# Optimization experiments

Measured on AMD Instinct MI355X. Metric: run time of the kernel, lower is better.

The kernel has to match this reference:

```python
import jax, jax.numpy as jnp
import numpy as np

NEG = -1e9

def conv1x1(x, w, b):
    # x: [B,C,H,W], w: [O,C], b: [O]
    return jnp.einsum('bchw,oc->bohw', x, w) + b[None, :, None, None]


def setup_inputs() -> dict:
    key = jax.random.key(0)
    ks = jax.random.split(key, 12)
    B, C, H, W = 4, 512, 96, 96
    Cr = min(8, C // 8)  # = 8
    s = lambda fan: 1.0 / np.sqrt(fan)
    inp = {
        'x':   jax.random.normal(ks[0], (B, C, H, W), dtype=jnp.float32),
        'w_h': jax.random.normal(ks[1], (Cr, C), dtype=jnp.float32) * s(C),
        'b_h': jax.random.normal(ks[2], (Cr,), dtype=jnp.float32) * s(C),
        'w_w': jax.random.normal(ks[3], (Cr, C), dtype=jnp.float32) * s(C),
        'b_w': jax.random.normal(ks[4], (Cr,), dtype=jnp.float32) * s(C),
        'w_c': jax.random.normal(ks[5], (C, C), dtype=jnp.float32) * s(C),
        'b_c': jax.random.normal(ks[6], (C,), dtype=jnp.float32) * s(C),
        'w_o': jax.random.normal(ks[7], (C, C), dtype=jnp.float32) * s(C),
        'b_o': jax.random.normal(ks[8], (C,), dtype=jnp.float32) * s(C),
        # alpha/beta/gamma are nn.Parameter(zeros(1)); use small nonzero values
        # so all branches contribute to output/gradients.
        'alpha': jax.random.normal(ks[9], (1,), dtype=jnp.float32) * 0.1,
        'beta':  jax.random.normal(ks[10], (1,), dtype=jnp.float32) * 0.1,
        'gamma': jax.random.normal(ks[11], (1,), dtype=jnp.float32) * 0.1,
    }
    return inp


def reference(x, w_h, b_h, w_w, b_w, w_c, b_c, w_o, b_o, alpha, beta, gamma):
    B, C, H, W = x.shape
    f_hei = conv1x1(x, w_h, b_h)              # [B,Cr,H,W]
    Cr = f_hei.shape[1]
    # Faithful replication of torch permute/contiguous/view sequence
    # (the .view(B*W,-1,H) after permute reinterprets the (H,Cr) layout as (Cr,H)).
    f_h = f_hei.transpose(0, 3, 2, 1).reshape(B * W, Cr, H).transpose(0, 2, 1)  # [B*W,H,Cr]
    f_w = f_hei.transpose(0, 2, 1, 3).reshape(B * H, Cr, W).transpose(0, 2, 1)  # [B*H,W,Cr]
    f_wid = conv1x1(x, w_w, b_w)              # [B,Cr,H,W]
    ff_h = f_wid.transpose(0, 3, 1, 2).reshape(B * W, Cr, H)  # [B*W,Cr,H]
    ff_w = f_wid.transpose(0, 2, 1, 3).reshape(B * H, Cr, W)  # [B*H,Cr,W]
    # channel attention branch
    f_ch = conv1x1(x, w_c, b_c)               # [B,C,H,W]
    f_c = f_ch.reshape(B, C, H * W)           # [B,C,HW]
    ff_c = f_ch.transpose(0, 2, 3, 1).reshape(B, H * W, C)    # [B,HW,C]
    aff_c = jax.nn.softmax(jnp.matmul(f_c, ff_c), axis=2)     # [B,C,C]
    out_C = jnp.matmul(ff_c, aff_c).reshape(B, C, H, W)       # torch .view reinterpretation
    # axial (criss-cross) attention with masked concat-softmax
    E_h = jnp.matmul(f_h, ff_h)               # [B*W,H,H]
    E_h = E_h + (jnp.eye(H, dtype=x.dtype) * NEG)[None, :, :]
    E_h = E_h.reshape(B, W, H, H).transpose(0, 2, 1, 3)       # [B,H,W,H]
    E_w = jnp.matmul(f_w, ff_w).reshape(B, H, W, W)           # [B,H,W,W]
    concate = jax.nn.softmax(jnp.concatenate([E_h, E_w], axis=3), axis=3)  # [B,H,W,H+W]
    h_att = concate[:, :, :, :H].transpose(0, 2, 1, 3).reshape(B * W, H, H)
    w_att = concate[:, :, :, H:].reshape(B * H, W, W)
    f_cha = conv1x1(x, w_o, b_o)              # [B,C,H,W]
    P_H = f_cha.transpose(0, 3, 1, 2).reshape(B * W, C, H)
    P_W = f_cha.transpose(0, 2, 1, 3).reshape(B * H, C, W)
    out_H = jnp.matmul(P_H, h_att.transpose(0, 2, 1)).reshape(B, W, C, H).transpose(0, 2, 3, 1)
    out_W = jnp.matmul(P_W, w_att.transpose(0, 2, 1)).reshape(B, H, C, W).transpose(0, 2, 1, 3)
    return x + alpha * out_H + beta * out_W + gamma * out_C
```

## Files before the change

kernel.cpp:

```cpp
#include <hip/hip_runtime.h>

typedef __attribute__((ext_vector_type(8))) short short8;
typedef __attribute__((ext_vector_type(4))) float f32x4;
typedef __attribute__((ext_vector_type(4))) unsigned short us4;
typedef unsigned short u16;

#define kB 4
#define kC 512
#define kCr 8
#define kH 96
#define kW 96
#define kHW 9216
#define kCHW 4718592
#define NEGV -1e9f

__device__ __forceinline__ u16 f2b(float f) {
  union { float f; unsigned u; } v; v.f = f;
  unsigned r = v.u + 0x7fff + ((v.u >> 16) & 1);
  return (u16)(r >> 16);
}
__device__ __forceinline__ float b2f(u16 h) {
  union { unsigned u; float f; } v; v.u = ((unsigned)h) << 16;
  return v.f;
}
#define MFMA(a, b, c) __builtin_amdgcn_mfma_f32_16x16x32_bf16(a, b, c, 0, 0, 0)

__device__ __forceinline__ void gl16(const u16* g, u16* l) {
  __builtin_amdgcn_global_load_lds(
      (const __attribute__((address_space(1))) void*)g,
      (__attribute__((address_space(3))) void*)l, 16, 0, 0);
}

__global__ __launch_bounds__(256) void k_cvt_T(const float* __restrict__ in,
                                               u16* __restrict__ out,
                                               int R, int C) {
  const float* ib = in + (size_t)blockIdx.z * R * C;
  u16* ob = out + (size_t)blockIdx.z * R * C;
  int c0 = blockIdx.x * 64, r0 = blockIdx.y * 64;
  __shared__ u16 T[64][68];
  int tid = threadIdx.x;
#pragma unroll
  for (int p = 0; p < 4; p++) {
    int ch = tid + p * 256;
    int i = ch >> 4, seg = ch & 15;
    f32x4 v = *(const f32x4*)&ib[(size_t)(r0 + i) * C + c0 + seg * 4];
    T[i][seg*4+0] = f2b(v[0]); T[i][seg*4+1] = f2b(v[1]);
    T[i][seg*4+2] = f2b(v[2]); T[i][seg*4+3] = f2b(v[3]);
  }
  __syncthreads();
#pragma unroll
  for (int p = 0; p < 4; p++) {
    int ch = tid + p * 256;
    int j = ch >> 4, seg = ch & 15;
    us4 o;
#pragma unroll
    for (int e = 0; e < 4; e++) o[e] = T[seg*4+e][j];
    *(us4*)&ob[(size_t)(c0 + j) * R + r0 + seg * 4] = o;
  }
}

__global__ __launch_bounds__(256) void k_trT_bf(const u16* __restrict__ in,
                                                u16* __restrict__ out,
                                                int R, int C) {
  const u16* ib = in + (size_t)blockIdx.z * R * C;
  u16* ob = out + (size_t)blockIdx.z * R * C;
  int c0 = blockIdx.x * 64, r0 = blockIdx.y * 64;
  __shared__ u16 T[64][68];
  int tid = threadIdx.x;
#pragma unroll
  for (int p = 0; p < 4; p++) {
    int ch = tid + p * 256;
    int i = ch >> 4, seg = ch & 15;
    us4 v = *(const us4*)&ib[(size_t)(r0 + i) * C + c0 + seg * 4];
    T[i][seg*4+0] = v[0]; T[i][seg*4+1] = v[1];
    T[i][seg*4+2] = v[2]; T[i][seg*4+3] = v[3];
  }
  __syncthreads();
#pragma unroll
  for (int p = 0; p < 4; p++) {
    int ch = tid + p * 256;
    int j = ch >> 4, seg = ch & 15;
    us4 o;
#pragma unroll
    for (int e = 0; e < 4; e++) o[e] = T[seg*4+e][j];
    *(us4*)&ob[(size_t)(c0 + j) * R + r0 + seg * 4] = o;
  }
}

__global__ __launch_bounds__(256) void k_cvtw(const float* __restrict__ wc,
                                              const float* __restrict__ wo,
                                              u16* __restrict__ wco) {
  int i = blockIdx.x * 256 + threadIdx.x;
  const float* src = (i < 65536) ? &wc[(size_t)i * 4] : &wo[(size_t)(i - 65536) * 4];
  f32x4 v = *(const f32x4*)src;
  us4 o;
  o[0] = f2b(v[0]); o[1] = f2b(v[1]); o[2] = f2b(v[2]); o[3] = f2b(v[3]);
  ((us4*)wco)[i] = o;
}

__global__ __launch_bounds__(256) void k_conv16(
    const float* __restrict__ wh, const float* __restrict__ bh,
    const float* __restrict__ ww, const float* __restrict__ bw,
    const u16* __restrict__ XT, u16* __restrict__ Out) {
  __shared__ u16 As[16][520];
  __shared__ float bias_s[16];
  int tid = threadIdx.x;
#pragma unroll
  for (int p = 0; p < 4; p++) {
    int ch = tid + p * 256;
    int r = ch >> 6, seg = ch & 63;
    const float* src = (r < 8) ? &wh[r * 512 + seg * 8] : &ww[(r - 8) * 512 + seg * 8];
    f32x4 v0 = *(const f32x4*)src;
    f32x4 v1 = *(const f32x4*)(src + 4);
    short8 sv;
    sv[0]=f2b(v0[0]); sv[1]=f2b(v0[1]); sv[2]=f2b(v0[2]); sv[3]=f2b(v0[3]);
    sv[4]=f2b(v1[0]); sv[5]=f2b(v1[1]); sv[6]=f2b(v1[2]); sv[7]=f2b(v1[3]);
    *(short8*)&As[r][seg * 8] = sv;
  }
  if (tid < 16) bias_s[tid] = (tid < 8) ? bh[tid] : bw[tid - 8];
  __syncthreads();
  int b = blockIdx.y;
  int nb = blockIdx.x * 128 + (tid >> 6) * 32;
  int lane = tid & 63;
  int lr = lane & 15, lg = lane >> 4;
  const u16* Bb = XT + (size_t)b * kCHW;
  f32x4 acc[2] = {};
#pragma unroll 4
  for (int k0 = 0; k0 < 512; k0 += 32) {
    short8 a = *(const short8*)&As[lr][k0 + lg * 8];
    short8 b0 = *(const short8*)&Bb[(size_t)(nb + lr) * 512 + k0 + lg * 8];
    short8 b1 = *(const short8*)&Bb[(size_t)(nb + 16 + lr) * 512 + k0 + lg * 8];
    acc[0] = MFMA(a, b0, acc[0]);
    acc[1] = MFMA(a, b1, acc[1]);
  }
#pragma unroll
  for (int q = 0; q < 2; q++)
#pragma unroll
    for (int r = 0; r < 4; r++) {
      int m = lg * 4 + r;
      Out[((size_t)b * 16 + m) * kHW + nb + q * 16 + lr] = f2b(acc[q][r] + bias_s[m]);
    }
}

#define GEMM_PROLOG()                                                      \
  int tid = threadIdx.x;                                                   \
  int lane = tid & 63, wv = tid >> 6;                                      \
  int wr = (wv >> 1) * 64, wc = (wv & 1) * 64;                             \
  int lr = lane & 15, lg = lane >> 4;                                      \
  f32x4 acc[4][4] = {};

#define STAGE(bufv, kk)                                                    \
  {                                                                        \
    _Pragma("unroll")                                                      \
    for (int p = 0; p < 4; p++) {                                          \
      int ch = tid + p * 256;                                              \
      int row = ch >> 3, cc = ch & 7;                                      \
      int sc = (cc ^ (row & 7)) * 8;                                       \
      gl16(&Asrc[(size_t)(bm + row) * LDA + (kk) + sc], &As[bufv][row][cc * 8]); \
      gl16(&Bsrc[(size_t)(bn + row) * LDB + (kk) + sc], &Bs[bufv][row][cc * 8]); \
    }                                                                      \
  }

#define COMPUTE(bufv)                                                      \
  {                                                                        \
    _Pragma("unroll")                                                      \
    for (int ks = 0; ks < 2; ks++) {                                       \
      int ca = ((ks * 4 + lg) ^ (lr & 7)) * 8;                             \
      short8 av[4], bv[4];                                                 \
      _Pragma("unroll")                                                    \
      for (int m = 0; m < 4; m++)                                          \
        av[m] = *(const short8*)&As[bufv][wr + m * 16 + lr][ca];           \
      _Pragma("unroll")                                                    \
      for (int n = 0; n < 4; n++)                                          \
        bv[n] = *(const short8*)&Bs[bufv][wc + n * 16 + lr][ca];           \
      _Pragma("unroll")                                                    \
      for (int m = 0; m < 4; m++)                                          \
        _Pragma("unroll")                                                  \
        for (int n = 0; n < 4; n++)                                        \
          acc[m][n] = MFMA(av[m], bv[n], acc[m][n]);                       \
    }                                                                      \
  }

__global__ __launch_bounds__(256) void k_gemm_conv2(
    const u16* __restrict__ wco, const u16* __restrict__ BT,
    const float* __restrict__ b_c, const float* __restrict__ b_o,
    u16* __restrict__ f_ch, u16* __restrict__ f_cha) {
  __shared__ u16 As[2][128][64];
  __shared__ u16 Bs[2][128][64];
  int b = blockIdx.z;
  int bm = blockIdx.y * 128;
  int bn = blockIdx.x * 128;
  const u16* Asrc = wco;
  const u16* Bsrc = BT + (size_t)b * kCHW;
  const int LDA = 512, LDB = 512;
  GEMM_PROLOG();
  STAGE(0, 0);
  __syncthreads();
  int cur = 0;
#pragma unroll 1
  for (int t = 0; t < 7; t++) {
    STAGE(cur ^ 1, (t + 1) * 64);
    COMPUTE(cur);
    __syncthreads();
    cur ^= 1;
  }
  COMPUTE(cur);
  const float* biasp = (bm < 512) ? (b_c + bm) : (b_o + bm - 512);
  u16* Ob = (bm < 512) ? (f_ch + (size_t)b * kCHW + (size_t)bm * kHW)
                       : (f_cha + (size_t)b * kCHW + (size_t)(bm - 512) * kHW);
#pragma unroll
  for (int m = 0; m < 4; m++)
#pragma unroll
    for (int r = 0; r < 4; r++) {
      int ol = wr + m * 16 + lg * 4 + r;
      float bv_ = biasp[ol];
#pragma unroll
      for (int n = 0; n < 4; n++)
        Ob[(size_t)ol * kHW + bn + wc + n * 16 + lr] = f2b(acc[m][n][r] + bv_);
    }
}

__global__ __launch_bounds__(256) void k_gram_sk(const u16* __restrict__ F,
                                                 float* __restrict__ part) {
  __shared__ u16 As[2][128][64];
  __shared__ u16 Bs[2][128][64];
  int z = blockIdx.z;
  int b = z & 3, s = z >> 2;
  int bm = blockIdx.y * 128, bn = blockIdx.x * 128;
  const u16* Asrc = F + (size_t)b * kCHW;
  const u16* Bsrc = Asrc;
  const int LDA = kHW, LDB = kHW;
  int kbeg = s * 1152;
  GEMM_PROLOG();
  STAGE(0, kbeg);
  __syncthreads();
  int cur = 0;
#pragma unroll 1
  for (int t = 0; t < 17; t++) {
    STAGE(cur ^ 1, kbeg + (t + 1) * 64);
    COMPUTE(cur);
    __syncthreads();
    cur ^= 1;
  }
  COMPUTE(cur);
  float* Pb = part + ((size_t)(s * 4 + b)) * 262144;
#pragma unroll
  for (int m = 0; m < 4; m++)
#pragma unroll
    for (int r = 0; r < 4; r++) {
      int i = bm + wr + m * 16 + lg * 4 + r;
#pragma unroll
      for (int n = 0; n < 4; n++)
        Pb[(size_t)i * 512 + bn + wc + n * 16 + lr] = acc[m][n][r];
    }
}

__global__ __launch_bounds__(256) void k_outc(
    const u16* __restrict__ AT, const u16* __restrict__ Bt,
    const float* __restrict__ gamma, u16* __restrict__ Out) {
  __shared__ u16 As[2][128][64];
  __shared__ u16 Bs[2][128][64];
  int b = blockIdx.z;
  int bm = blockIdx.y * 128;
  int bn = blockIdx.x * 128;
  const u16* Asrc = AT + (size_t)b * kCHW;
  const u16* Bsrc = Bt + (size_t)b * 262144;
  const int LDA = 512, LDB = 512;
  GEMM_PROLOG();
  STAGE(0, 0);
  __syncthreads();
  int cur = 0;
#pragma unroll 1
  for (int t = 0; t < 7; t++) {
    STAGE(cur ^ 1, (t + 1) * 64);
    COMPUTE(cur);
    __syncthreads();
    cur ^= 1;
  }
  COMPUTE(cur);
  float g = *gamma;
  u16* Ob = Out + (size_t)b * kCHW;
#pragma unroll
  for (int m = 0; m < 4; m++)
#pragma unroll
    for (int r = 0; r < 4; r++) {
      int mm = bm + wr + m * 16 + lg * 4 + r;
#pragma unroll
      for (int n = 0; n < 4; n++)
        Ob[(size_t)mm * 512 + bn + wc + n * 16 + lr] = f2b(g * acc[m][n][r]);
    }
}

__global__ __launch_bounds__(256) void k_softmax512r(const float* __restrict__ part,
                                                     float* __restrict__ gramN) {
  int b = blockIdx.x >> 9, i = blockIdx.x & 511;
  int tid = threadIdx.x;
  float v0 = 0.f, v1 = 0.f;
#pragma unroll
  for (int s = 0; s < 8; s++) {
    const float* P = part + ((size_t)(s * 4 + b) * 512 + i) * 512;
    v0 += P[tid];
    v1 += P[tid + 256];
  }
  int wid = tid >> 6, lane = tid & 63;
  float m = fmaxf(v0, v1);
#pragma unroll
  for (int o = 32; o >= 1; o >>= 1) m = fmaxf(m, __shfl_xor(m, o));
  __shared__ float redm[4], reds[4];
  if (lane == 0) redm[wid] = m;
  __syncthreads();
  m = fmaxf(fmaxf(redm[0], redm[1]), fmaxf(redm[2], redm[3]));
  float e0 = expf(v0 - m), e1 = expf(v1 - m);
  float s = e0 + e1;
#pragma unroll
  for (int o = 32; o >= 1; o >>= 1) s += __shfl_xor(s, o);
  if (lane == 0) reds[wid] = s;
  __syncthreads();
  s = reds[0] + reds[1] + reds[2] + reds[3];
  float inv = 1.0f / s;
  float* R = gramN + ((size_t)b * 512 + i) * 512;
  R[tid] = e0 * inv;
  R[tid + 256] = e1 * inv;
}

__global__ __launch_bounds__(256) void k_eh(
    const u16* __restrict__ fhw, u16* __restrict__ Ccat) {
  int b = blockIdx.x / kW, w = blockIdx.x % kW;
  __shared__ float fh[kH][kCr];
  __shared__ float fw[kCr][kH];
  int tid = threadIdx.x;
  for (int l = tid; l < kH * kCr; l += 256) {
    int i = l >> 3, c = l & 7;
    fh[i][c] = b2f(fhw[((size_t)b * 16 + (i & 7)) * kHW + (c * 12 + (i >> 3)) * kW + w]);
    int c2 = l / kH, j = l % kH;
    fw[c2][j] = b2f(fhw[((size_t)b * 16 + 8 + c2) * kHW + j * kW + w]);
  }
  __syncthreads();
  for (int t = tid; t < kH * kH; t += 256) {
    int i = t / kH, j = t % kH;
    float e = 0.f;
#pragma unroll
    for (int c = 0; c < kCr; c++) e += fh[i][c] * fw[c][j];
    if (i == j) e += NEGV;
    Ccat[(((size_t)b * kH + i) * kW + w) * 192 + j] = f2b(e);
  }
}

__global__ __launch_bounds__(256) void k_ew(
    const u16* __restrict__ fhw, u16* __restrict__ Ccat) {
  int b = blockIdx.x / kH, h = blockIdx.x % kH;
  __shared__ float fh2[kCr][kW];
  __shared__ float fw2[kCr][kW];
  int tid = threadIdx.x;
  for (int l = tid; l < kCr * kW; l += 256) {
    int c = l / kW, w = l % kW;
    fh2[c][w] = b2f(fhw[((size_t)b * 16 + c) * kHW + h * kW + w]);
    fw2[c][w] = b2f(fhw[((size_t)b * 16 + 8 + c) * kHW + h * kW + w]);
  }
  __syncthreads();
  for (int t = tid; t < kW * kW; t += 256) {
    int w = t / kW, j = t % kW;
    float e = 0.f;
#pragma unroll
    for (int c = 0; c < kCr; c++) e += fh2[c][w] * fw2[c][j];
    Ccat[(((size_t)b * kH + h) * kW + w) * 192 + 96 + j] = f2b(e);
  }
}

__global__ __launch_bounds__(256) void k_softmax192(u16* __restrict__ Ccat) {
  int r = blockIdx.x * 4 + (threadIdx.x >> 6);
  int lane = threadIdx.x & 63;
  u16* R = Ccat + (size_t)r * 192;
  float a = b2f(R[lane]), b = b2f(R[lane + 64]), c = b2f(R[lane + 128]);
  float m = fmaxf(a, fmaxf(b, c));
#pragma unroll
  for (int o = 32; o >= 1; o >>= 1) m = fmaxf(m, __shfl_xor(m, o));
  float ea = expf(a - m), eb = expf(b - m), ec = expf(c - m);
  float s = ea + eb + ec;
#pragma unroll
  for (int o = 32; o >= 1; o >>= 1) s += __shfl_xor(s, o);
  float inv = 1.0f / s;
  R[lane] = f2b(ea * inv);
  R[lane + 64] = f2b(eb * inv);
  R[lane + 128] = f2b(ec * inv);
}

__global__ __launch_bounds__(256) void k_tr_plane(const u16* __restrict__ in,
                                                  u16* __restrict__ out) {
  size_t pl = blockIdx.x;
  const u16* ib = in + pl * 9216;
  u16* ob = out + pl * 9216;
  __shared__ u16 T[96][100];
  int tid = threadIdx.x;
  for (int ch = tid; ch < 96 * 24; ch += 256) {
    int i = ch / 24, seg = ch % 24;
    *(us4*)&T[i][seg*4] = *(const us4*)&ib[i*96 + seg*4];
  }
  __syncthreads();
  for (int ch = tid; ch < 96 * 24; ch += 256) {
    int j = ch / 24, seg = ch % 24;
    us4 o;
#pragma unroll
    for (int e = 0; e < 4; e++) o[e] = T[seg*4+e][j];
    *(us4*)&ob[j*96 + seg*4] = o;
  }
}

__global__ __launch_bounds__(512) void k_final_h(
    const u16* __restrict__ AT,
    const u16* __restrict__ att,
    const float* __restrict__ alpha,
    u16* __restrict__ OutHT) {
  int b = blockIdx.x / 96, w = blockIdx.x % 96;
  __shared__ u16 Bs[96][104];
  int tid = threadIdx.x;
  for (int ch = tid; ch < 1152; ch += 512) {
    int h = ch / 12, seg = ch % 12;
    *(short8*)&Bs[h][seg*8] =
        *(const short8*)&att[(((size_t)b*96 + h)*96 + w)*192 + seg*8];
  }
  __syncthreads();
  int lane = tid & 63, wv = tid >> 6;
  int lr = lane & 15, lg = lane >> 4;
  int c0 = wv * 64;
  const u16* Ab = AT + ((size_t)b*512 + c0)*kHW + w*96;
  f32x4 acc[4][6] = {};
#pragma unroll
  for (int ks = 0; ks < 3; ks++) {
    short8 av[4];
#pragma unroll
    for (int m = 0; m < 4; m++)
      av[m] = *(const short8*)&Ab[(size_t)(m*16 + lr)*kHW + ks*32 + lg*8];
#pragma unroll
    for (int n = 0; n < 6; n++) {
      short8 bv = *(const short8*)&Bs[n*16 + lr][ks*32 + lg*8];
#pragma unroll
      for (int m = 0; m < 4; m++) acc[m][n] = MFMA(av[m], bv, acc[m][n]);
    }
  }
  float al = *alpha;
  u16* Ob = OutHT + ((size_t)b*512 + c0)*kHW + w*96;
#pragma unroll
  for (int m = 0; m < 4; m++)
#pragma unroll
    for (int r = 0; r < 4; r++) {
      size_t crow = (size_t)(m*16 + lg*4 + r) * kHW;
#pragma unroll
      for (int n = 0; n < 6; n++)
        Ob[crow + n*16 + lr] = f2b(al * acc[m][n][r]);
    }
}

__global__ __launch_bounds__(512) void k_final_w(
    const u16* __restrict__ A,
    const u16* __restrict__ att,
    const float* __restrict__ beta,
    u16* __restrict__ OutW) {
  int b = blockIdx.x / 96, h = blockIdx.x % 96;
  __shared__ u16 Bs[96][104];
  int tid = threadIdx.x;
  for (int ch = tid; ch < 1152; ch += 512) {
    int wr_ = ch / 12, seg = ch % 12;
    *(short8*)&Bs[wr_][seg*8] =
        *(const short8*)&att[(((size_t)b*96 + h)*96 + wr_)*192 + 96 + seg*8];
  }
  __syncthreads();
  int lane = tid & 63, wv = tid >> 6;
  int lr = lane & 15, lg = lane >> 4;
  int c0 = wv * 64;
  const u16* Ab = A + ((size_t)b*512 + c0)*kHW + h*96;
  f32x4 acc[4][6] = {};
#pragma unroll
  for (int ks = 0; ks < 3; ks++) {
    short8 av[4];
#pragma unroll
    for (int m = 0; m < 4; m++)
      av[m] = *(const short8*)&Ab[(size_t)(m*16 + lr)*kHW + ks*32 + lg*8];
#pragma unroll
    for (int n = 0; n < 6; n++) {
      short8 bv = *(const short8*)&Bs[n*16 + lr][ks*32 + lg*8];
#pragma unroll
      for (int m = 0; m < 4; m++) acc[m][n] = MFMA(av[m], bv, acc[m][n]);
    }
  }
  float be = *beta;
  u16* Ob = OutW + ((size_t)b*512 + c0)*kHW + h*96;
#pragma unroll
  for (int m = 0; m < 4; m++)
#pragma unroll
    for (int r = 0; r < 4; r++) {
      size_t crow = (size_t)(m*16 + lg*4 + r) * kHW;
#pragma unroll
      for (int n = 0; n < 6; n++)
        Ob[crow + n*16 + lr] = f2b(be * acc[m][n][r]);
    }
}

__global__ __launch_bounds__(256) void k_merge(
    const float* __restrict__ x, const u16* __restrict__ OutC,
    const u16* __restrict__ OutW, const u16* __restrict__ HT,
    float* __restrict__ out) {
  size_t pl = blockIdx.x;
  const u16* hb = HT + pl * 9216;
  __shared__ u16 T[96][100];
  int tid = threadIdx.x;
  for (int ch = tid; ch < 96 * 24; ch += 256) {
    int i = ch / 24, seg = ch % 24;
    *(us4*)&T[i][seg*4] = *(const us4*)&hb[i*96 + seg*4];
  }
  __syncthreads();
  const float* xb = x + pl * 9216;
  const u16* cb = OutC + pl * 9216;
  const u16* wb = OutW + pl * 9216;
  float* ob = out + pl * 9216;
  for (int ch = tid; ch < 2304; ch += 256) {
    int i4 = ch * 4;
    int h = i4 / 96, w = i4 % 96;
    f32x4 xv = *(const f32x4*)&xb[i4];
    us4 cv = *(const us4*)&cb[i4];
    us4 wv = *(const us4*)&wb[i4];
    f32x4 o;
#pragma unroll
    for (int e = 0; e < 4; e++)
      o[e] = xv[e] + b2f(cv[e]) + b2f(wv[e]) + b2f(T[w + e][h]);
    *(f32x4*)&ob[i4] = o;
  }
}

extern "C" void kernel_launch(void* const* d_in, const int* in_sizes, int n_in,
                              void* d_out, int out_size, void* d_ws, size_t ws_size,
                              hipStream_t stream) {
  const float* x     = (const float*)d_in[0];
  const float* w_h   = (const float*)d_in[1];
  const float* b_h   = (const float*)d_in[2];
  const float* w_w   = (const float*)d_in[3];
  const float* b_w   = (const float*)d_in[4];
  const float* w_c   = (const float*)d_in[5];
  const float* b_c   = (const float*)d_in[6];
  const float* w_o   = (const float*)d_in[7];
  const float* b_o   = (const float*)d_in[8];
  const float* alpha = (const float*)d_in[9];
  const float* beta  = (const float*)d_in[10];
  const float* gamma = (const float*)d_in[11];
  float* out = (float*)d_out;

  const size_t R = 37748736;
  char* p = (char*)d_ws;
  u16*   xbfT   = (u16*)(p);
  float* part   = (float*)(p);
  u16*   f_chaT = (u16*)(p);
  u16*   outW   = (u16*)(p);
  u16*   f_ch   = (u16*)(p + R);
  u16*   outC   = (u16*)(p + R);
  u16*   f_chT  = (u16*)(p + 2 * R);
  u16*   outHT  = (u16*)(p + 2 * R);
  u16*   f_cha  = (u16*)(p + 3 * R);
  u16*   fhw    = (u16*)(p + 4 * R);
  char*  F      = p + 4 * R + 2359296;
  float* gramN  = (float*)F;
  u16*   affT   = (u16*)(F + 4194304);
  u16*   ccat   = (u16*)F;
  u16*   wco    = (u16*)(F + 14155776);

  k_cvt_T<<<dim3(144, 8, 4), 256, 0, stream>>>(x, xbfT, 512, 9216);
  k_cvtw<<<512, 256, 0, stream>>>(w_c, w_o, wco);
  k_conv16<<<dim3(72, 4), 256, 0, stream>>>(w_h, b_h, w_w, b_w, xbfT, fhw);
  k_gemm_conv2<<<dim3(72, 8, 4), 256, 0, stream>>>(wco, xbfT, b_c, b_o, f_ch, f_cha);
  k_trT_bf<<<dim3(144, 8, 4), 256, 0, stream>>>(f_ch, f_chT, 512, 9216);
  k_gram_sk<<<dim3(4, 4, 32), 256, 0, stream>>>(f_ch, part);
  k_softmax512r<<<2048, 256, 0, stream>>>(part, gramN);
  k_cvt_T<<<dim3(8, 8, 4), 256, 0, stream>>>(gramN, affT, 512, 512);
  k_outc<<<dim3(4, 72, 4), 256, 0, stream>>>(f_chT, affT, gamma, outC);
  k_eh<<<384, 256, 0, stream>>>(fhw, ccat);
  k_ew<<<384, 256, 0, stream>>>(fhw, ccat);
  k_softmax192<<<9216, 256, 0, stream>>>(ccat);
  k_tr_plane<<<2048, 256, 0, stream>>>(f_cha, f_chaT);
  k_final_h<<<384, 512, 0, stream>>>(f_chaT, ccat, alpha, outHT);
  k_final_w<<<384, 512, 0, stream>>>(f_cha, ccat, beta, outW);
  k_merge<<<2048, 256, 0, stream>>>(x, outC, outW, outHT, out);
}
```

Measured before the change: 310.7 us.

## Deepen GEMM load pipeline with vmcnt waits and store gram partials in bf16

Restructures the shared-memory GEMM main loop to prefetch two K-tiles ahead and wait with explicit vmcnt/lgkmcnt counters plus raw barriers, instead of a full sync each iteration. MFMA sections are wrapped in raised wave priority. The split-K gram partial sums are now written and read as bf16 instead of fp32, which halves that intermediate traffic. The cost is reduced precision in the summed partials before the softmax, and the hand-written wait counts must match the number of loads per stage.

```diff
diff --git a/kernel.cpp b/kernel.cpp
--- a/kernel.cpp
+++ b/kernel.cpp
@@ -173,12 +173,42 @@
       _Pragma("unroll")                                                    \
       for (int n = 0; n < 4; n++)                                          \
         bv[n] = *(const short8*)&Bs[bufv][wc + n * 16 + lr][ca];           \
+      __builtin_amdgcn_s_setprio(1);                                       \
       _Pragma("unroll")                                                    \
       for (int m = 0; m < 4; m++)                                          \
         _Pragma("unroll")                                                  \
         for (int n = 0; n < 4; n++)                                        \
           acc[m][n] = MFMA(av[m], bv[n], acc[m][n]);                       \
+      __builtin_amdgcn_s_setprio(0);                                       \
     }                                                                      \
+  }
+
+#define VMBAR(N)                                                           \
+  asm volatile("s_waitcnt vmcnt(" #N ")" ::: "memory");                    \
+  __builtin_amdgcn_s_barrier();
+
+#define LGBAR                                                              \
+  asm volatile("s_waitcnt lgkmcnt(0)" ::: "memory");                       \
+  __builtin_amdgcn_s_barrier();
+
+#define PIPELOOP(NT, KBASE)                                                \
+  STAGE(0, (KBASE));                                                       \
+  STAGE(1, (KBASE) + 64);                                                  \
+  {                                                                        \
+    int cur = 0;                                                           \
+    _Pragma("unroll 1")                                                    \
+    for (int t = 0; t < (NT) - 2; t++) {                                   \
+      VMBAR(8);                                                            \
+      COMPUTE(cur);                                                        \
+      LGBAR;                                                               \
+      STAGE(cur, (KBASE) + (t + 2) * 64);                                  \
+      cur ^= 1;                                                            \
+    }                                                                      \
+    VMBAR(8);                                                              \
+    COMPUTE(cur);                                                          \
+    cur ^= 1;                                                              \
+    VMBAR(0);                                                              \
+    COMPUTE(cur);                                                          \
   }
 
 __global__ __launch_bounds__(256) void k_gemm_conv2(
@@ -194,17 +224,7 @@
   const u16* Bsrc = BT + (size_t)b * kCHW;
   const int LDA = 512, LDB = 512;
   GEMM_PROLOG();
-  STAGE(0, 0);
-  __syncthreads();
-  int cur = 0;
-#pragma unroll 1
-  for (int t = 0; t < 7; t++) {
-    STAGE(cur ^ 1, (t + 1) * 64);
-    COMPUTE(cur);
-    __syncthreads();
-    cur ^= 1;
-  }
-  COMPUTE(cur);
+  PIPELOOP(8, 0);
   const float* biasp = (bm < 512) ? (b_c + bm) : (b_o + bm - 512);
   u16* Ob = (bm < 512) ? (f_ch + (size_t)b * kCHW + (size_t)bm * kHW)
                        : (f_cha + (size_t)b * kCHW + (size_t)(bm - 512) * kHW);
@@ -221,7 +241,7 @@
 }
 
 __global__ __launch_bounds__(256) void k_gram_sk(const u16* __restrict__ F,
-                                                 float* __restrict__ part) {
+                                                 u16* __restrict__ part) {
   __shared__ u16 As[2][128][64];
   __shared__ u16 Bs[2][128][64];
   int z = blockIdx.z;
@@ -232,18 +252,8 @@
   const int LDA = kHW, LDB = kHW;
   int kbeg = s * 1152;
   GEMM_PROLOG();
-  STAGE(0, kbeg);
-  __syncthreads();
-  int cur = 0;
-#pragma unroll 1
-  for (int t = 0; t < 17; t++) {
-    STAGE(cur ^ 1, kbeg + (t + 1) * 64);
-    COMPUTE(cur);
-    __syncthreads();
-    cur ^= 1;
-  }
-  COMPUTE(cur);
-  float* Pb = part + ((size_t)(s * 4 + b)) * 262144;
+  PIPELOOP(18, kbeg);
+  u16* Pb = part + ((size_t)(s * 4 + b)) * 262144;
 #pragma unroll
   for (int m = 0; m < 4; m++)
 #pragma unroll
@@ -251,7 +261,7 @@
       int i = bm + wr + m * 16 + lg * 4 + r;
 #pragma unroll
       for (int n = 0; n < 4; n++)
-        Pb[(size_t)i * 512 + bn + wc + n * 16 + lr] = acc[m][n][r];
+        Pb[(size_t)i * 512 + bn + wc + n * 16 + lr] = f2b(acc[m][n][r]);
     }
 }
 
@@ -267,17 +277,7 @@
   const u16* Bsrc = Bt + (size_t)b * 262144;
   const int LDA = 512, LDB = 512;
   GEMM_PROLOG();
-  STAGE(0, 0);
-  __syncthreads();
-  int cur = 0;
-#pragma unroll 1
-  for (int t = 0; t < 7; t++) {
-    STAGE(cur ^ 1, (t + 1) * 64);
-    COMPUTE(cur);
-    __syncthreads();
-    cur ^= 1;
-  }
-  COMPUTE(cur);
+  PIPELOOP(8, 0);
   float g = *gamma;
   u16* Ob = Out + (size_t)b * kCHW;
 #pragma unroll
@@ -291,16 +291,16 @@
     }
 }
 
-__global__ __launch_bounds__(256) void k_softmax512r(const float* __restrict__ part,
+__global__ __launch_bounds__(256) void k_softmax512r(const u16* __restrict__ part,
                                                      float* __restrict__ gramN) {
   int b = blockIdx.x >> 9, i = blockIdx.x & 511;
   int tid = threadIdx.x;
   float v0 = 0.f, v1 = 0.f;
 #pragma unroll
   for (int s = 0; s < 8; s++) {
-    const float* P = part + ((size_t)(s * 4 + b) * 512 + i) * 512;
-    v0 += P[tid];
-    v1 += P[tid + 256];
+    const u16* P = part + ((size_t)(s * 4 + b) * 512 + i) * 512;
+    v0 += b2f(P[tid]);
+    v1 += b2f(P[tid + 256]);
   }
   int wid = tid >> 6, lane = tid & 63;
   float m = fmaxf(v0, v1);
@@ -547,7 +547,7 @@
   const size_t R = 37748736;
   char* p = (char*)d_ws;
   u16*   xbfT   = (u16*)(p);
-  float* part   = (float*)(p);
+  u16*   part   = (u16*)(p);
   u16*   f_chaT = (u16*)(p);
   u16*   outW   = (u16*)(p);
   u16*   f_ch   = (u16*)(p + R);
```

Result: no change. 304.9 us (-1.9%).
